# Optimization experiments

Hardware: AMD Instinct MI355X
Metric: run time of the kernel (lower is better)

Reference implementation:

```python
import jax, jax.numpy as jnp
import numpy as np

H = 1024
N_HEAD = 16
HEAD = H // N_HEAD
EPS = 1e-12


def setup_inputs() -> dict:
    key = jax.random.key(0)
    ks = jax.random.split(key, 12)
    B, S = 2, 2048
    scale = 1.0 / np.sqrt(H)
    inp = {
        "pre_out": jax.random.normal(ks[0], (B, S, H), dtype=jnp.float32),
        "att_mask": jnp.ones((B, 1, 1, S), dtype=jnp.float32),
        "Wq": jax.random.normal(ks[1], (H, H), dtype=jnp.float32) * scale,
        "bq": jnp.zeros((H,), dtype=jnp.float32),
        "Wk": jax.random.normal(ks[2], (H, H), dtype=jnp.float32) * scale,
        "bk": jnp.zeros((H,), dtype=jnp.float32),
        "Wv": jax.random.normal(ks[3], (H, H), dtype=jnp.float32) * scale,
        "bv": jnp.zeros((H,), dtype=jnp.float32),
        "Wo": jax.random.normal(ks[4], (H, H), dtype=jnp.float32) * scale,
        "bo": jnp.zeros((H,), dtype=jnp.float32),
        "ln_w": jnp.ones((H,), dtype=jnp.float32),
        "ln_b": jnp.zeros((H,), dtype=jnp.float32),
    }
    return inp


def _heads(x):
    # [B,S,H] -> [B,n_head,S,head]
    B, S, _ = x.shape
    return x.reshape(B, S, N_HEAD, HEAD).transpose(0, 2, 1, 3)


def _layernorm(x, w, b):
    u = jnp.mean(x, axis=-1, keepdims=True)
    s = jnp.mean((x - u) ** 2, axis=-1, keepdims=True)
    return w * ((x - u) / jnp.sqrt(s + EPS)) + b


def reference(pre_out, att_mask, Wq, bq, Wk, bk, Wv, bv, Wo, bo, ln_w, ln_b):
    B, S, _ = pre_out.shape
    # torch Linear: y = x @ W.T + b
    Q = _heads(pre_out @ Wq.T + bq)
    K = _heads(pre_out @ Wk.T + bk)
    V = _heads(pre_out @ Wv.T + bv)
    scores = jnp.einsum('bhqd,bhkd->bhqk', Q, K) / np.sqrt(HEAD)
    scores = scores + (1.0 - att_mask) * -10000.0
    prob = jax.nn.softmax(scores, axis=-1)  # eval mode: no dropout
    att = jnp.einsum('bhqk,bhkd->bhqd', prob, V)
    att = att.transpose(0, 2, 1, 3).reshape(B, S, H)
    out = att @ Wo.T + bo
    return _layernorm(pre_out + out, ln_w, ln_b)
```

## Files before the change

### kernel.cpp

```cpp
#include <hip/hip_runtime.h>
#include <math.h>

typedef unsigned short u16;
typedef float floatx4 __attribute__((ext_vector_type(4)));
typedef __bf16 bf16x8 __attribute__((ext_vector_type(8)));
typedef u16 u16x4 __attribute__((ext_vector_type(4)));

#define BB 2
#define SS 2048
#define HH 1024
#define NHEAD 16

__device__ __forceinline__ u16 f2bf(float f) {
  union { float f; unsigned u; } a; a.f = f;
  unsigned r = a.u + 0x7fffu + ((a.u >> 16) & 1u);
  return (u16)(r >> 16);
}

__device__ __forceinline__ u16 bfbits(float f) {
  union { __bf16 h; u16 u; } c; c.h = (__bf16)f; return c.u;
}

__device__ __forceinline__ void gload16(const u16* g, u16* l) {
  __builtin_amdgcn_global_load_lds((const __attribute__((address_space(1))) void*)g,
                                   (__attribute__((address_space(3))) void*)l, 16, 0, 0);
}

__device__ __forceinline__ void fencebar() {
  asm volatile("" ::: "memory");
  __builtin_amdgcn_s_barrier();
  asm volatile("" ::: "memory");
}

__global__ __launch_bounds__(256) void cvt_all(
    const float* __restrict__ X, const float* __restrict__ Wq, const float* __restrict__ Wk,
    const float* __restrict__ Wv, const float* __restrict__ Wo, const float* __restrict__ mask,
    u16* __restrict__ Xb, u16* __restrict__ Wqb, u16* __restrict__ Wkb,
    u16* __restrict__ Wvb, u16* __restrict__ Wob, float* __restrict__ B2) {
  int i = blockIdx.x * 256 + threadIdx.x;
  if (i >= (2 << 20)) {
    int off = i - (2 << 20);
    float4 m = ((const float4*)mask)[off];
    float4 o;
    o.x = (1.0f - m.x) * (-10000.0f * 1.44269504f);
    o.y = (1.0f - m.y) * (-10000.0f * 1.44269504f);
    o.z = (1.0f - m.z) * (-10000.0f * 1.44269504f);
    o.w = (1.0f - m.w) * (-10000.0f * 1.44269504f);
    ((float4*)B2)[off] = o;
    return;
  }
  const float* src; u16* dst; int off;
  if (i < (1 << 20)) { src = X; dst = Xb; off = i; }
  else {
    int j = i - (1 << 20);
    int m = j >> 18; off = j & ((1 << 18) - 1);
    src = (m == 0) ? Wq : (m == 1) ? Wk : (m == 2) ? Wv : Wo;
    dst = (m == 0) ? Wqb : (m == 1) ? Wkb : (m == 2) ? Wvb : Wob;
  }
  float4 v = ((const float4*)src)[off];
  u16x4 p; p.x = f2bf(v.x); p.y = f2bf(v.y); p.z = f2bf(v.z); p.w = f2bf(v.w);
  ((u16x4*)dst)[off] = p;
}

__global__ __launch_bounds__(256) void qkv_gemm(
    const u16* __restrict__ X,
    const u16* __restrict__ Wq, const u16* __restrict__ Wk, const u16* __restrict__ Wv,
    const float* __restrict__ bq, const float* __restrict__ bk, const float* __restrict__ bv,
    u16* __restrict__ Qo, u16* __restrict__ Ko, u16* __restrict__ Vt) {
  __shared__ u16 As[128 * 32];
  __shared__ u16 Ws[128 * 32];

  const int tid = threadIdx.x;
  const int w = tid >> 6, lane = tid & 63, quad = lane >> 4, l15 = lane & 15;
  const int L = blockIdx.y * 24 + blockIdx.x;
  const int wid = (L & 7) * 96 + (L >> 3);
  const int bx = wid % 24, by = wid / 24;
  const int mat = bx >> 3;
  const int col0 = (bx & 7) * 128;
  const int row0 = by * 128;
  const u16* W = (mat == 0) ? Wq : (mat == 1) ? Wk : Wv;
  const float* bias = (mat == 0) ? bq : (mat == 1) ? bk : bv;

  const int c0 = tid, c1 = tid + 256;
  const int ar0 = c0 >> 2, al0 = ((c0 & 3) ^ (ar0 & 3)) * 8;
  const int ar1 = c1 >> 2, al1 = ((c1 & 3) ^ (ar1 & 3)) * 8;
  const u16* gA0 = X + (row0 + ar0) * HH + al0;
  const u16* gA1 = X + (row0 + ar1) * HH + al1;
  const u16* gW0 = W + (col0 + ar0) * HH + al0;
  const u16* gW1 = W + (col0 + ar1) * HH + al1;
  u16* lA0 = As + c0 * 8; u16* lA1 = As + c1 * 8;
  u16* lW0 = Ws + c0 * 8; u16* lW1 = Ws + c1 * 8;

  const int wm = (w >> 1) * 64, wn = (w & 1) * 64;
  const int sw = quad ^ (l15 & 3);
  const int aoff = (wm + l15) * 32 + sw * 8;
  const int boff = (wn + l15) * 32 + sw * 8;

  floatx4 acc[4][4];
#pragma unroll
  for (int i = 0; i < 4; i++)
#pragma unroll
    for (int j = 0; j < 4; j++) acc[i][j] = {0.f, 0.f, 0.f, 0.f};

  for (int k0 = 0; k0 < HH; k0 += 32) {
    __syncthreads();
    gload16(gA0 + k0, lA0);
    gload16(gA1 + k0, lA1);
    gload16(gW0 + k0, lW0);
    gload16(gW1 + k0, lW1);
    __syncthreads();
    bf16x8 af[4], bfr[4];
#pragma unroll
    for (int i = 0; i < 4; i++) af[i] = *(const bf16x8*)(As + aoff + i * 512);
#pragma unroll
    for (int j = 0; j < 4; j++) bfr[j] = *(const bf16x8*)(Ws + boff + j * 512);
#pragma unroll
    for (int i = 0; i < 4; i++)
#pragma unroll
      for (int j = 0; j < 4; j++)
        acc[i][j] = __builtin_amdgcn_mfma_f32_16x16x32_bf16(af[i], bfr[j], acc[i][j], 0, 0, 0);
  }

  const int rb = row0 + wm + quad * 4;
  if (mat < 2) {
    u16* O = (mat == 0) ? Qo : Ko;
#pragma unroll
    for (int j = 0; j < 4; j++) {
      const int col = col0 + wn + j * 16 + l15;
      const float bj = bias[col];
#pragma unroll
      for (int i = 0; i < 4; i++) {
        const int r0 = rb + i * 16;
#pragma unroll
        for (int r = 0; r < 4; r++)
          O[(r0 + r) * HH + col] = bfbits(acc[i][j][r] + bj);
      }
    }
  } else {
#pragma unroll
    for (int j = 0; j < 4; j++) {
      const int col = col0 + wn + j * 16 + l15;
      const float bj = bias[col];
      const int h = col >> 6, d = col & 63;
#pragma unroll
      for (int i = 0; i < 4; i++) {
        const int m0 = rb + i * 16;
        const int b = m0 >> 11, s = m0 & 2047;
        u16x4 pk;
#pragma unroll
        for (int r = 0; r < 4; r++) pk[r] = bfbits(acc[i][j][r] + bj);
        *(u16x4*)(Vt + (((b * NHEAD + h) * 64 + d) * SS + s)) = pk;
      }
    }
  }
}

__global__ __launch_bounds__(256) void oproj_gemm(
    const u16* __restrict__ A, const u16* __restrict__ W,
    const float* __restrict__ bias, float* __restrict__ Y) {
  __shared__ u16 As[128 * 32];
  __shared__ u16 Ws[64 * 32];

  const int tid = threadIdx.x;
  const int w = tid >> 6, lane = tid & 63, quad = lane >> 4, l15 = lane & 15;
  const int L = blockIdx.y * 16 + blockIdx.x;
  const int wid = (L & 7) * 64 + (L >> 3);
  const int col0 = (wid & 15) * 64;
  const int row0 = (wid >> 4) * 128;

  const int c0 = tid, c1 = tid + 256;
  const int ar0 = c0 >> 2, al0 = ((c0 & 3) ^ (ar0 & 3)) * 8;
  const int ar1 = c1 >> 2, al1 = ((c1 & 3) ^ (ar1 & 3)) * 8;
  const u16* gA0 = A + (row0 + ar0) * HH + al0;
  const u16* gA1 = A + (row0 + ar1) * HH + al1;
  const u16* gW0 = W + (col0 + ar0) * HH + al0;
  u16* lA0 = As + c0 * 8; u16* lA1 = As + c1 * 8;
  u16* lW0 = Ws + c0 * 8;

  const int wm = w * 32;
  const int sw = quad ^ (l15 & 3);
  const int aoff = (wm + l15) * 32 + sw * 8;
  const int boff = l15 * 32 + sw * 8;

  floatx4 acc[2][4];
#pragma unroll
  for (int i = 0; i < 2; i++)
#pragma unroll
    for (int j = 0; j < 4; j++) acc[i][j] = {0.f, 0.f, 0.f, 0.f};

  for (int k0 = 0; k0 < HH; k0 += 32) {
    __syncthreads();
    gload16(gA0 + k0, lA0);
    gload16(gA1 + k0, lA1);
    if (tid < 256) gload16(gW0 + k0, lW0);
    __syncthreads();
    bf16x8 af[2], bfr[4];
#pragma unroll
    for (int i = 0; i < 2; i++) af[i] = *(const bf16x8*)(As + aoff + i * 512);
#pragma unroll
    for (int j = 0; j < 4; j++) bfr[j] = *(const bf16x8*)(Ws + boff + j * 512);
#pragma unroll
    for (int i = 0; i < 2; i++)
#pragma unroll
      for (int j = 0; j < 4; j++)
        acc[i][j] = __builtin_amdgcn_mfma_f32_16x16x32_bf16(af[i], bfr[j], acc[i][j], 0, 0, 0);
  }

  const int rb = row0 + wm + quad * 4;
#pragma unroll
  for (int j = 0; j < 4; j++) {
    const int col = col0 + j * 16 + l15;
    const float bj = bias[col];
#pragma unroll
    for (int i = 0; i < 2; i++) {
      const int r0 = rb + i * 16;
#pragma unroll
      for (int r = 0; r < 4; r++)
        Y[(r0 + r) * HH + col] = acc[i][j][r] + bj;
    }
  }
}

#define QT 128

__global__ __launch_bounds__(512, 4) void attn_mfma(
    const u16* __restrict__ Q, const u16* __restrict__ K, const u16* __restrict__ Vt,
    const float* __restrict__ B2, u16* __restrict__ O) {
  __shared__ u16 SMEM[26624];
  u16* const UQ = SMEM;
  u16* const KS0 = SMEM + 10240;
  u16* const KS1 = SMEM + 14336;
  u16* const VS0 = SMEM + 18432;
  u16* const VS1 = SMEM + 22528;

  const int L = blockIdx.y * 16 + blockIdx.x;
  const int wid = (L & 7) * 64 + (L >> 3);
  const int qt = wid & 15, bh = wid >> 4;
  const int b = bh >> 4, h = bh & 15;
  const int tid = threadIdx.x;
  const int w = tid >> 6, lane = tid & 63, quad = lane >> 4, l15 = lane & 15;
  const int sw = l15 & 7;
  const int qg = w & 3;
  const int khalf = w >> 2;
  const int koff = khalf * 32;
  const int kh4 = khalf * 4;

  const int qbase  = (b * SS + qt * QT) * HH + h * 64;
  const int kvbase = (b * SS) * HH + h * 64;
  const int vtbase = (b * NHEAD + h) * 64 * SS;

  auto stage_kv = [&](u16* kd, u16* vd, int t) {
    const int c = tid;
    const int r = c >> 3, lc = (c & 7) ^ (r & 7);
    gload16(K + kvbase + (t * 64 + r) * HH + lc * 8, kd + c * 8);
    gload16(Vt + vtbase + r * SS + t * 64 + lc * 8, vd + c * 8);
  };

#pragma unroll
  for (int i = 0; i < 2; i++) {
    const int c = tid + i * 512;
    const int r = c >> 3, lc = (c & 7) ^ (r & 7);
    gload16(Q + qbase + r * HH + lc * 8, UQ + c * 8);
  }
  stage_kv(KS0, VS0, 0);
  asm volatile("s_waitcnt vmcnt(2)" ::: "memory");
  fencebar();

  bf16x8 aQ[2][2];
#pragma unroll
  for (int mt = 0; mt < 2; mt++) {
    const u16* qr = UQ + (qg * 32 + mt * 16 + l15) * 64;
    aQ[mt][0] = *(const bf16x8*)(qr + ((quad ^ sw) * 8));
    aQ[mt][1] = *(const bf16x8*)(qr + (((4 + quad) ^ sw) * 8));
  }
  asm volatile("s_waitcnt lgkmcnt(0)" ::: "memory");

  floatx4 o[2][4];
#pragma unroll
  for (int mt = 0; mt < 2; mt++)
#pragma unroll
    for (int j = 0; j < 4; j++) o[mt][j] = {0.f, 0.f, 0.f, 0.f};
  float lp[2] = {0.f, 0.f};

  u16* const Pw = UQ + w * 1280;
  const float* B2row = B2 + b * SS;

  for (int kt = 0; kt < 32; kt++) {
    const int cur = kt & 1;
    const u16* Kc = cur ? KS1 : KS0;
    const u16* Vc = cur ? VS1 : VS0;

    const float* B2k = B2row + kt * 64 + koff;
    floatx4 bb[2];
    bb[0] = *(const floatx4*)(B2k + quad * 4);
    bb[1] = *(const floatx4*)(B2k + 16 + quad * 4);
    asm volatile("" ::: "memory");

    if (kt < 31) {
      stage_kv(cur ? KS0 : KS1, cur ? VS0 : VS1, kt + 1);
      asm volatile("s_waitcnt vmcnt(2)" ::: "memory");
    } else {
      asm volatile("s_waitcnt vmcnt(0)" ::: "memory");
    }
    fencebar();

    floatx4 st[2][2];
    __builtin_amdgcn_s_setprio(1);
#pragma unroll
    for (int kb = 0; kb < 2; kb++) {
      const u16* kr = Kc + (koff + kb * 16 + l15) * 64;
      bf16x8 kf0 = *(const bf16x8*)(kr + ((quad ^ sw) * 8));
      bf16x8 kf1 = *(const bf16x8*)(kr + (((4 + quad) ^ sw) * 8));
#pragma unroll
      for (int mt = 0; mt < 2; mt++) {
        floatx4 z = {0.f, 0.f, 0.f, 0.f};
        z = __builtin_amdgcn_mfma_f32_16x16x32_bf16(kf0, aQ[mt][0], z, 0, 0, 0);
        st[mt][kb] = __builtin_amdgcn_mfma_f32_16x16x32_bf16(kf1, aQ[mt][1], z, 0, 0, 0);
      }
    }
    __builtin_amdgcn_s_setprio(0);

#pragma unroll
    for (int kb = 0; kb < 2; kb++) {
#pragma unroll
      for (int mt = 0; mt < 2; mt++) {
        u16x4 pk;
#pragma unroll
        for (int r = 0; r < 4; r++) {
          const float p = __builtin_amdgcn_exp2f(st[mt][kb][r] * 0.180336880f + bb[kb][r]);
          lp[mt] += p;
          pk[r] = bfbits(p);
        }
        *(u16x4*)(Pw + (mt * 16 + l15) * 40 + kb * 16 + quad * 4) = pk;
      }
    }

    bf16x8 pa[2];
#pragma unroll
    for (int mt = 0; mt < 2; mt++)
      pa[mt] = *(const bf16x8*)(Pw + (mt * 16 + l15) * 40 + quad * 8);
    __builtin_amdgcn_s_setprio(1);
#pragma unroll
    for (int j = 0; j < 4; j++) {
      const u16* vr = Vc + (j * 16 + l15) * 64;
      bf16x8 vf = *(const bf16x8*)(vr + (((kh4 + quad) ^ sw) * 8));
#pragma unroll
      for (int mt = 0; mt < 2; mt++)
        o[mt][j] = __builtin_amdgcn_mfma_f32_16x16x32_bf16(pa[mt], vf, o[mt][j], 0, 0, 0);
    }
    __builtin_amdgcn_s_setprio(0);

    fencebar();
  }

#pragma unroll
  for (int mt = 0; mt < 2; mt++) {
    float v = lp[mt];
    v += __shfl_xor(v, 16);
    v += __shfl_xor(v, 32);
    lp[mt] = v;
  }

  float* const oS  = (float*)(SMEM + 10240);
  float* const lpS = (float*)SMEM;
  if (w >= 4) {
    float* pb = oS + (w - 4) * 2048;
#pragma unroll
    for (int mt = 0; mt < 2; mt++) {
#pragma unroll
      for (int j = 0; j < 4; j++)
#pragma unroll
        for (int r = 0; r < 4; r++)
          pb[(mt * 16 + quad * 4 + r) * 64 + j * 16 + l15] = o[mt][j][r];
      if (quad == 0) lpS[qg * 32 + mt * 16 + l15] = lp[mt];
    }
  }
  asm volatile("s_waitcnt lgkmcnt(0)" ::: "memory");
  fencebar();

  if (w < 4) {
    const float* pb = oS + w * 2048;
    float lpt[2];
#pragma unroll
    for (int mt = 0; mt < 2; mt++)
      lpt[mt] = lp[mt] + lpS[w * 32 + mt * 16 + l15];
#pragma unroll
    for (int mt = 0; mt < 2; mt++) {
      const int orow0 = b * SS + qt * QT + qg * 32 + mt * 16 + quad * 4;
#pragma unroll
      for (int r = 0; r < 4; r++) {
        const float inv = 1.0f / __shfl(lpt[mt], quad * 4 + r);
#pragma unroll
        for (int j = 0; j < 4; j++) {
          const float val = o[mt][j][r] + pb[(mt * 16 + quad * 4 + r) * 64 + j * 16 + l15];
          O[(orow0 + r) * HH + h * 64 + j * 16 + l15] = bfbits(val * inv);
        }
      }
    }
  }
}

__device__ __forceinline__ float block_sum256(float v) {
  __shared__ float sb[4];
#pragma unroll
  for (int o = 1; o < 64; o <<= 1) v += __shfl_xor(v, o);
  if ((threadIdx.x & 63) == 0) sb[threadIdx.x >> 6] = v;
  __syncthreads();
  float r = sb[0] + sb[1] + sb[2] + sb[3];
  __syncthreads();
  return r;
}

__global__ __launch_bounds__(256) void add_layernorm(
    const float* __restrict__ x0, const float* __restrict__ y,
    const float* __restrict__ w, const float* __restrict__ b,
    float* __restrict__ out) {
  const int row = blockIdx.x;
  const int t = threadIdx.x;
  const float* xr = x0 + (size_t)row * HH;
  const float* yr = y + (size_t)row * HH;

  float v[4];
  float sum = 0.f;
#pragma unroll
  for (int i = 0; i < 4; i++) {
    int idx = t + i * 256;
    v[i] = xr[idx] + yr[idx];
    sum += v[i];
  }
  float mean = block_sum256(sum) * (1.0f / HH);

  float sq = 0.f;
#pragma unroll
  for (int i = 0; i < 4; i++) {
    float d = v[i] - mean;
    sq += d * d;
  }
  float var = block_sum256(sq) * (1.0f / HH);
  float inv = rsqrtf(var + 1e-12f);

#pragma unroll
  for (int i = 0; i < 4; i++) {
    int idx = t + i * 256;
    out[(size_t)row * HH + idx] = w[idx] * ((v[i] - mean) * inv) + b[idx];
  }
}

extern "C" void kernel_launch(void* const* d_in, const int* in_sizes, int n_in,
                              void* d_out, int out_size, void* d_ws, size_t ws_size,
                              hipStream_t stream) {
  const float* pre_out = (const float*)d_in[0];
  const float* mask    = (const float*)d_in[1];
  const float* Wq = (const float*)d_in[2];
  const float* bq = (const float*)d_in[3];
  const float* Wk = (const float*)d_in[4];
  const float* bk = (const float*)d_in[5];
  const float* Wv = (const float*)d_in[6];
  const float* bv = (const float*)d_in[7];
  const float* Wo = (const float*)d_in[8];
  const float* bo = (const float*)d_in[9];
  const float* ln_w = (const float*)d_in[10];
  const float* ln_b = (const float*)d_in[11];
  float* out = (float*)d_out;

  u16* Xb  = (u16*)d_ws;
  u16* Wqb = Xb + (4 << 20);
  u16* Wkb = Wqb + (1 << 20);
  u16* Wvb = Wkb + (1 << 20);
  u16* Wob = Wvb + (1 << 20);
  u16* Qb  = Wob + (1 << 20);
  u16* Kb  = Qb + (4 << 20);
  u16* Vtb = Kb + (4 << 20);
  u16* Ab  = Vtb + (4 << 20);
  float* Yb = (float*)(Ab + (4 << 20));
  float* B2 = Yb + (4 << 20);

  cvt_all<<<8196, 256, 0, stream>>>(pre_out, Wq, Wk, Wv, Wo, mask,
                                    Xb, Wqb, Wkb, Wvb, Wob, B2);

  qkv_gemm<<<dim3(24, 32), 256, 0, stream>>>(Xb, Wqb, Wkb, Wvb, bq, bk, bv, Qb, Kb, Vtb);

  attn_mfma<<<dim3(SS / QT, BB * NHEAD), 512, 0, stream>>>(Qb, Kb, Vtb, B2, Ab);

  oproj_gemm<<<dim3(16, 32), 256, 0, stream>>>(Ab, Wob, bo, Yb);

  add_layernorm<<<BB * SS, 256, 0, stream>>>(pre_out, Yb, ln_w, ln_b, out);
}
```

Baseline: 202.8 us.

## Double-buffer LDS tiles in QKV and output-projection GEMMs

Both projection GEMMs now keep two LDS buffers and issue the async global-to-LDS loads for the next K tile before computing on the current one. Partial vmcnt waits and barriers replace the two full syncs per iteration, so load latency can overlap with MFMA work. It also raises wave priority around the MFMA block. The cost is doubled LDS per block, which may reduce occupancy. It also depends on fencebar being defined elsewhere and on the vmcnt counts matching the number of loads in flight.

```diff
diff --git a/kernel.cpp b/kernel.cpp
--- a/kernel.cpp
+++ b/kernel.cpp
@@ -67,8 +67,8 @@
     const u16* __restrict__ Wq, const u16* __restrict__ Wk, const u16* __restrict__ Wv,
     const float* __restrict__ bq, const float* __restrict__ bk, const float* __restrict__ bv,
     u16* __restrict__ Qo, u16* __restrict__ Ko, u16* __restrict__ Vt) {
-  __shared__ u16 As[128 * 32];
-  __shared__ u16 Ws[128 * 32];
+  __shared__ u16 As[2][128 * 32];
+  __shared__ u16 Ws[2][128 * 32];
 
   const int tid = threadIdx.x;
   const int w = tid >> 6, lane = tid & 63, quad = lane >> 4, l15 = lane & 15;
@@ -88,37 +88,51 @@
   const u16* gA1 = X + (row0 + ar1) * HH + al1;
   const u16* gW0 = W + (col0 + ar0) * HH + al0;
   const u16* gW1 = W + (col0 + ar1) * HH + al1;
-  u16* lA0 = As + c0 * 8; u16* lA1 = As + c1 * 8;
-  u16* lW0 = Ws + c0 * 8; u16* lW1 = Ws + c1 * 8;
 
   const int wm = (w >> 1) * 64, wn = (w & 1) * 64;
   const int sw = quad ^ (l15 & 3);
   const int aoff = (wm + l15) * 32 + sw * 8;
   const int boff = (wn + l15) * 32 + sw * 8;
 
+  auto stage = [&](int buf, int k0) {
+    gload16(gA0 + k0, As[buf] + c0 * 8);
+    gload16(gA1 + k0, As[buf] + c1 * 8);
+    gload16(gW0 + k0, Ws[buf] + c0 * 8);
+    gload16(gW1 + k0, Ws[buf] + c1 * 8);
+  };
+
   floatx4 acc[4][4];
 #pragma unroll
   for (int i = 0; i < 4; i++)
 #pragma unroll
     for (int j = 0; j < 4; j++) acc[i][j] = {0.f, 0.f, 0.f, 0.f};
 
-  for (int k0 = 0; k0 < HH; k0 += 32) {
-    __syncthreads();
-    gload16(gA0 + k0, lA0);
-    gload16(gA1 + k0, lA1);
-    gload16(gW0 + k0, lW0);
-    gload16(gW1 + k0, lW1);
-    __syncthreads();
+  stage(0, 0);
+
+  for (int kt = 0; kt < 32; kt++) {
+    const int cur = kt & 1;
+    if (kt < 31) {
+      stage(cur ^ 1, (kt + 1) * 32);
+      asm volatile("s_waitcnt vmcnt(4)" ::: "memory");
+    } else {
+      asm volatile("s_waitcnt vmcnt(0)" ::: "memory");
+    }
+    fencebar();
+
     bf16x8 af[4], bfr[4];
 #pragma unroll
-    for (int i = 0; i < 4; i++) af[i] = *(const bf16x8*)(As + aoff + i * 512);
-#pragma unroll
-    for (int j = 0; j < 4; j++) bfr[j] = *(const bf16x8*)(Ws + boff + j * 512);
+    for (int i = 0; i < 4; i++) af[i] = *(const bf16x8*)(As[cur] + aoff + i * 512);
+#pragma unroll
+    for (int j = 0; j < 4; j++) bfr[j] = *(const bf16x8*)(Ws[cur] + boff + j * 512);
+    __builtin_amdgcn_s_setprio(1);
 #pragma unroll
     for (int i = 0; i < 4; i++)
 #pragma unroll
       for (int j = 0; j < 4; j++)
         acc[i][j] = __builtin_amdgcn_mfma_f32_16x16x32_bf16(af[i], bfr[j], acc[i][j], 0, 0, 0);
+    __builtin_amdgcn_s_setprio(0);
+
+    fencebar();
   }
 
   const int rb = row0 + wm + quad * 4;
@@ -158,8 +172,8 @@
 __global__ __launch_bounds__(256) void oproj_gemm(
     const u16* __restrict__ A, const u16* __restrict__ W,
     const float* __restrict__ bias, float* __restrict__ Y) {
-  __shared__ u16 As[128 * 32];
-  __shared__ u16 Ws[64 * 32];
+  __shared__ u16 As[2][128 * 32];
+  __shared__ u16 Ws[2][64 * 32];
 
   const int tid = threadIdx.x;
   const int w = tid >> 6, lane = tid & 63, quad = lane >> 4, l15 = lane & 15;
@@ -174,36 +188,50 @@
   const u16* gA0 = A + (row0 + ar0) * HH + al0;
   const u16* gA1 = A + (row0 + ar1) * HH + al1;
   const u16* gW0 = W + (col0 + ar0) * HH + al0;
-  u16* lA0 = As + c0 * 8; u16* lA1 = As + c1 * 8;
-  u16* lW0 = Ws + c0 * 8;
 
   const int wm = w * 32;
   const int sw = quad ^ (l15 & 3);
   const int aoff = (wm + l15) * 32 + sw * 8;
   const int boff = l15 * 32 + sw * 8;
 
+  auto stage = [&](int buf, int k0) {
+    gload16(gA0 + k0, As[buf] + c0 * 8);
+    gload16(gA1 + k0, As[buf] + c1 * 8);
+    gload16(gW0 + k0, Ws[buf] + c0 * 8);
+  };
+
   floatx4 acc[2][4];
 #pragma unroll
   for (int i = 0; i < 2; i++)
 #pragma unroll
     for (int j = 0; j < 4; j++) acc[i][j] = {0.f, 0.f, 0.f, 0.f};
 
-  for (int k0 = 0; k0 < HH; k0 += 32) {
-    __syncthreads();
-    gload16(gA0 + k0, lA0);
-    gload16(gA1 + k0, lA1);
-    if (tid < 256) gload16(gW0 + k0, lW0);
-    __syncthreads();
+  stage(0, 0);
+
+  for (int kt = 0; kt < 32; kt++) {
+    const int cur = kt & 1;
+    if (kt < 31) {
+      stage(cur ^ 1, (kt + 1) * 32);
+      asm volatile("s_waitcnt vmcnt(3)" ::: "memory");
+    } else {
+      asm volatile("s_waitcnt vmcnt(0)" ::: "memory");
+    }
+    fencebar();
+
     bf16x8 af[2], bfr[4];
 #pragma unroll
-    for (int i = 0; i < 2; i++) af[i] = *(const bf16x8*)(As + aoff + i * 512);
-#pragma unroll
-    for (int j = 0; j < 4; j++) bfr[j] = *(const bf16x8*)(Ws + boff + j * 512);
+    for (int i = 0; i < 2; i++) af[i] = *(const bf16x8*)(As[cur] + aoff + i * 512);
+#pragma unroll
+    for (int j = 0; j < 4; j++) bfr[j] = *(const bf16x8*)(Ws[cur] + boff + j * 512);
+    __builtin_amdgcn_s_setprio(1);
 #pragma unroll
     for (int i = 0; i < 2; i++)
 #pragma unroll
       for (int j = 0; j < 4; j++)
         acc[i][j] = __builtin_amdgcn_mfma_f32_16x16x32_bf16(af[i], bfr[j], acc[i][j], 0, 0, 0);
+    __builtin_amdgcn_s_setprio(0);
+
+    fencebar();
   }
 
   const int rb = row0 + wm + quad * 4;
```

Result: slower. 208.9 us (+3.0%).
